# Optimization experiments

Measured on AMD Instinct MI355X. Metric: run time of the kernel, lower is better.

The kernel has to match this reference:

```python
import jax, jax.numpy as jnp
import numpy as np

T = 8192
H = 512
OUT = 2


def _lstm_layer(x, h0, c0, W_ih, W_hh, b_ih, b_hh):
    """Unidirectional LSTM layer, PyTorch gate order (i, f, g, o).
    x: (T, H_in); h0, c0: (H,). Returns (T, H) hidden sequence."""
    b = b_ih + b_hh  # (4H,)
    # Precompute input projections for all timesteps in one GEMM: (T, 4H)
    xg = x @ W_ih.T + b

    def step(carry, xgt):
        h, c = carry
        g = xgt + h @ W_hh.T  # (4H,)
        i, f, gg, o = jnp.split(g, 4)
        i = jax.nn.sigmoid(i)
        f = jax.nn.sigmoid(f)
        gg = jnp.tanh(gg)
        o = jax.nn.sigmoid(o)
        c = f * c + i * gg
        h = o * jnp.tanh(c)
        return (h, c), h

    (_, _), hs = jax.lax.scan(step, (h0, c0), xg)
    return hs


def setup_inputs() -> dict:
    key = jax.random.key(0)
    ks = jax.random.split(key, 16)
    bound = 1.0 / np.sqrt(H)

    def u(k, shape):
        return jax.random.uniform(k, shape, jnp.float32, -bound, bound)

    inp = {
        "tensor_data": jax.random.normal(ks[0], (T, 1, H), jnp.float32),
        "truth_v": jax.random.uniform(ks[1], (T, 1, OUT), jnp.float32),
        "h0": jax.random.normal(ks[2], (2, 1, H), jnp.float32),
        "c0": jax.random.normal(ks[3], (2, 1, H), jnp.float32),
        # layer 0 LSTM params (PyTorch layout: weight_ih (4H, H_in))
        "W_ih0": u(ks[4], (4 * H, H)),
        "W_hh0": u(ks[5], (4 * H, H)),
        "b_ih0": u(ks[6], (4 * H,)),
        "b_hh0": u(ks[7], (4 * H,)),
        # layer 1 LSTM params
        "W_ih1": u(ks[8], (4 * H, H)),
        "W_hh1": u(ks[9], (4 * H, H)),
        "b_ih1": u(ks[10], (4 * H,)),
        "b_hh1": u(ks[11], (4 * H,)),
        # linear head
        "W_head": u(ks[12], (OUT, H)),
        "b_head": u(ks[13], (OUT,)),
    }
    return inp


def reference(tensor_data, truth_v, h0, c0,
              W_ih0, W_hh0, b_ih0, b_hh0,
              W_ih1, W_hh1, b_ih1, b_hh1,
              W_head, b_head):
    x = tensor_data[:, 0, :]  # (T, H), batch = 1
    h1 = _lstm_layer(x, h0[0, 0], c0[0, 0], W_ih0, W_hh0, b_ih0, b_hh0)
    h2 = _lstm_layer(h1, h0[1, 0], c0[1, 0], W_ih1, W_hh1, b_ih1, b_hh1)
    logits = h2 @ W_head.T + b_head  # (T, OUT)
    p = jax.nn.sigmoid(logits)
    y = truth_v[:, 0, :]
    # BCELoss (mean reduction); clamp logs at -100 like torch.nn.BCELoss
    log_p = jnp.maximum(jnp.log(p), -100.0)
    log_1mp = jnp.maximum(jnp.log1p(-p), -100.0)
    loss = -jnp.mean(y * log_p + (1.0 - y) * log_1mp)
    return loss
```

## Files before the change

### kernel.cpp

```cpp
#include <hip/hip_runtime.h>
#include <stdint.h>

#define TSTEPS 8192
#define HDIM 512

typedef unsigned long long ull;

__device__ __forceinline__ ull pack_th(unsigned tag, float v) {
    union { float f; unsigned u; } x; x.f = v;
    return ((ull)tag << 32) | (ull)x.u;
}
__device__ __forceinline__ float unpack_v(ull p) {
    union { unsigned u; float f; } x; x.u = (unsigned)p;
    return x.f;
}

__global__ __attribute__((amdgpu_waves_per_eu(1, 1))) __launch_bounds__(256)
void lstm_fused(
    const float* __restrict__ x,
    const float* __restrict__ Whh0,
    const float* __restrict__ Wih0,
    const float* __restrict__ bih0,
    const float* __restrict__ bhh0,
    const float* __restrict__ Wih1,
    const float* __restrict__ Whh1,
    const float* __restrict__ bih1,
    const float* __restrict__ bhh1,
    const float* __restrict__ h0,
    const float* __restrict__ c0,
    float* __restrict__ h2seq,
    ull* __restrict__ ring0,
    ull* __restrict__ ring1)
{
    const int L2   = (blockIdx.x >= 128) ? 1 : 0;
    const int wb   = L2 ? (int)blockIdx.x - 128 : (int)blockIdx.x;
    const int tid  = threadIdx.x;
    const int wave = tid >> 6;
    const int lane = tid & 63;
    const int j    = wb * 4 + wave;

    float wA[4][8], wB[4][8];
    {
        const float* WA = L2 ? Whh1 : Whh0;
        const float* WB = L2 ? Wih1 : Wih0;
#pragma unroll
        for (int r = 0; r < 4; ++r) {
            const size_t rb = (size_t)(r * HDIM + j) * HDIM + lane;
#pragma unroll
            for (int u = 0; u < 8; ++u) {
                wA[r][u] = WA[rb + 64 * u];
                wB[r][u] = WB[rb + 64 * u];
            }
        }
    }
    float bb[4];
#pragma unroll
    for (int r = 0; r < 4; ++r)
        bb[r] = L2 ? (bih1[r * HDIM + j] + bhh1[r * HDIM + j])
                   : (bih0[r * HDIM + j] + bhh0[r * HDIM + j]);
    float c = c0[(L2 ? HDIM : 0) + j];

    ull* rring = L2 ? ring1 : ring0;

    if (lane == 0)
        __hip_atomic_store(&rring[j], pack_th(1u, h0[(L2 ? HDIM : 0) + j]),
                           __ATOMIC_RELAXED, __HIP_MEMORY_SCOPE_AGENT);

    float fv[8];
    if (!L2) {
#pragma unroll
        for (int u = 0; u < 8; ++u) fv[u] = x[lane + 64 * u];
    } else {
        const ull* s = ring0 + (size_t)1 * HDIM + lane;
        ull p[8]; bool ok;
        do {
            ok = true;
#pragma unroll
            for (int u = 0; u < 8; ++u)
                p[u] = __hip_atomic_load(&s[64 * u], __ATOMIC_RELAXED, __HIP_MEMORY_SCOPE_AGENT);
#pragma unroll
            for (int u = 0; u < 8; ++u) ok &= ((unsigned)(p[u] >> 32) == 2u);
            if (!ok) __builtin_amdgcn_s_sleep(1);
        } while (!ok);
#pragma unroll
        for (int u = 0; u < 8; ++u) fv[u] = unpack_v(p[u]);
    }

    for (int t = 0; t < TSTEPS; ++t) {
        float hv[8];
        {
            const ull* s = rring + (size_t)t * HDIM + lane;
            const unsigned tg = (unsigned)(t + 1);
            ull p[8]; bool ok;
            do {
                ok = true;
#pragma unroll
                for (int u = 0; u < 8; ++u)
                    p[u] = __hip_atomic_load(&s[64 * u], __ATOMIC_RELAXED, __HIP_MEMORY_SCOPE_AGENT);
#pragma unroll
                for (int u = 0; u < 8; ++u) ok &= ((unsigned)(p[u] >> 32) == tg);
                if (!ok) __builtin_amdgcn_s_sleep(1);
            } while (!ok);
#pragma unroll
            for (int u = 0; u < 8; ++u) hv[u] = unpack_v(p[u]);
        }

        float a0 = 0.f, a1 = 0.f, a2 = 0.f, a3 = 0.f;
#pragma unroll
        for (int u = 0; u < 8; ++u) {
            a0 += wA[0][u] * hv[u]; a1 += wA[1][u] * hv[u];
            a2 += wA[2][u] * hv[u]; a3 += wA[3][u] * hv[u];
        }
#pragma unroll
        for (int u = 0; u < 8; ++u) {
            a0 += wB[0][u] * fv[u]; a1 += wB[1][u] * fv[u];
            a2 += wB[2][u] * fv[u]; a3 += wB[3][u] * fv[u];
        }

#pragma unroll
        for (int m = 1; m < 64; m <<= 1) {
            a0 += __shfl_xor(a0, m);
            a1 += __shfl_xor(a1, m);
            a2 += __shfl_xor(a2, m);
            a3 += __shfl_xor(a3, m);
        }

        const float iv = 1.f / (1.f + __expf(-(a0 + bb[0])));
        const float ff = 1.f / (1.f + __expf(-(a1 + bb[1])));
        const float gg = 1.f - 2.f / (__expf(2.f * (a2 + bb[2])) + 1.f);
        const float ov = 1.f / (1.f + __expf(-(a3 + bb[3])));
        c = ff * c + iv * gg;
        const float h = ov * (1.f - 2.f / (__expf(2.f * c) + 1.f));

        if (lane == 0)
            __hip_atomic_store(&rring[(size_t)(t + 1) * HDIM + j],
                               pack_th((unsigned)(t + 2), h),
                               __ATOMIC_RELAXED, __HIP_MEMORY_SCOPE_AGENT);
        if (L2 && lane == 1)
            h2seq[(size_t)t * HDIM + j] = h;

        if (t + 1 < TSTEPS) {
            if (!L2) {
#pragma unroll
                for (int u = 0; u < 8; ++u)
                    fv[u] = x[(size_t)(t + 1) * HDIM + lane + 64 * u];
            } else {
                const ull* s = ring0 + (size_t)(t + 2) * HDIM + lane;
                const unsigned tg = (unsigned)(t + 3);
                ull p[8]; bool ok;
                do {
                    ok = true;
#pragma unroll
                    for (int u = 0; u < 8; ++u)
                        p[u] = __hip_atomic_load(&s[64 * u], __ATOMIC_RELAXED, __HIP_MEMORY_SCOPE_AGENT);
#pragma unroll
                    for (int u = 0; u < 8; ++u) ok &= ((unsigned)(p[u] >> 32) == tg);
                    if (!ok) __builtin_amdgcn_s_sleep(1);
                } while (!ok);
#pragma unroll
                for (int u = 0; u < 8; ++u) fv[u] = unpack_v(p[u]);
            }
        }
    }
}

__global__ __launch_bounds__(256) void head_loss(
    const float* __restrict__ h2,
    const float* __restrict__ Wh,
    const float* __restrict__ bh,
    const float* __restrict__ y,
    float* __restrict__ out)
{
    const int tid  = threadIdx.x;
    const int lane = tid & 63;
    const int wv   = tid >> 6;
    const int gw   = blockIdx.x * 4 + wv;

    float w0[8], w1[8];
#pragma unroll
    for (int u = 0; u < 8; ++u) {
        w0[u] = Wh[lane * 8 + u];
        w1[u] = Wh[HDIM + lane * 8 + u];
    }

    float lsum = 0.f;
    for (int t = gw; t < TSTEPS; t += 1024) {
        const float* hp = h2 + (size_t)t * HDIM + lane * 8;
        float4 hv0 = *(const float4*)&hp[0];
        float4 hv1 = *(const float4*)&hp[4];
        float a0 = hv0.x * w0[0] + hv0.y * w0[1] + hv0.z * w0[2] + hv0.w * w0[3]
                 + hv1.x * w0[4] + hv1.y * w0[5] + hv1.z * w0[6] + hv1.w * w0[7];
        float a1 = hv0.x * w1[0] + hv0.y * w1[1] + hv0.z * w1[2] + hv0.w * w1[3]
                 + hv1.x * w1[4] + hv1.y * w1[5] + hv1.z * w1[6] + hv1.w * w1[7];
#pragma unroll
        for (int m = 1; m < 64; m <<= 1) {
            a0 += __shfl_xor(a0, m);
            a1 += __shfl_xor(a1, m);
        }
        if (lane == 0) {
            const float z0 = a0 + bh[0];
            const float z1 = a1 + bh[1];
            const float p0 = 1.f / (1.f + __expf(-z0));
            const float p1 = 1.f / (1.f + __expf(-z1));
            const float lp0  = fmaxf(__logf(p0), -100.f);
            const float lp1  = fmaxf(__logf(p1), -100.f);
            const float l1p0 = fmaxf(log1pf(-p0), -100.f);
            const float l1p1 = fmaxf(log1pf(-p1), -100.f);
            const float y0 = y[(size_t)t * 2 + 0];
            const float y1 = y[(size_t)t * 2 + 1];
            lsum += y0 * lp0 + (1.f - y0) * l1p0;
            lsum += y1 * lp1 + (1.f - y1) * l1p1;
        }
    }

    __shared__ float red[4];
    if (lane == 0) red[wv] = lsum;
    __syncthreads();
    if (tid == 0) {
        const float ssum = red[0] + red[1] + red[2] + red[3];
        atomicAdd(out, ssum * (-1.f / (float)(TSTEPS * 2)));
    }
}

extern "C" void kernel_launch(void* const* d_in, const int* in_sizes, int n_in,
                              void* d_out, int out_size, void* d_ws, size_t ws_size,
                              hipStream_t stream)
{
    const float* x     = (const float*)d_in[0];
    const float* truth = (const float*)d_in[1];
    const float* h0    = (const float*)d_in[2];
    const float* c0    = (const float*)d_in[3];
    const float* Wih0  = (const float*)d_in[4];
    const float* Whh0  = (const float*)d_in[5];
    const float* bih0  = (const float*)d_in[6];
    const float* bhh0  = (const float*)d_in[7];
    const float* Wih1  = (const float*)d_in[8];
    const float* Whh1  = (const float*)d_in[9];
    const float* bih1  = (const float*)d_in[10];
    const float* bhh1  = (const float*)d_in[11];
    const float* Whead = (const float*)d_in[12];
    const float* bhead = (const float*)d_in[13];

    char* ws = (char*)d_ws;
    ull*   ring0 = (ull*)ws;
    ull*   ring1 = (ull*)(ws + (((size_t)34) << 20));
    float* h2seq = (float*)(ws + (((size_t)68) << 20));

    hipMemsetAsync(d_out, 0, (size_t)out_size * sizeof(float), stream);

    lstm_fused<<<256, 256, 0, stream>>>(x, Whh0, Wih0, bih0, bhh0,
                                        Wih1, Whh1, bih1, bhh1,
                                        h0, c0, h2seq, ring0, ring1);
    head_loss<<<256, 256, 0, stream>>>(h2seq, Whead, bhead, truth, (float*)d_out);
}
```

Baseline: 15.43 ms.

## Restructure LSTM kernel: 64 active blocks, LDS-resident input weights, dual-ring fast polling

Reworks the persistent LSTM kernel so that only 2 of every 8 blocks stay active (one per layer). This is meant to spread the active blocks across separate XCDs or CUs. Each block now handles 16 hidden units, with 16 lanes per unit, and the input-weight slice lives in LDS. The h vector is staged through LDS and broadcast with __syncthreads, and the input-projection partial sum is computed before waiting on the recurrent h. Each h is published to two rings: one read by a fast sc0 vector-load spin without sleeps, and an agent-scope atomic ring used as a fallback. The aim is to shorten the per-step cross-block synchronization latency, at the cost of extra stores, block barriers, and reliance on cache-coherence behaviour of the sc0 path.

```diff
diff --git a/kernel.cpp b/kernel.cpp
--- a/kernel.cpp
+++ b/kernel.cpp
@@ -3,8 +3,12 @@
 
 #define TSTEPS 8192
 #define HDIM 512
+#define LDS_BYTES 135168
+#define WARM 32
+#define FASTK 4096
 
 typedef unsigned long long ull;
+typedef unsigned int uint4v __attribute__((ext_vector_type(4)));
 
 __device__ __forceinline__ ull pack_th(unsigned tag, float v) {
     union { float f; unsigned u; } x; x.f = v;
@@ -14,44 +18,77 @@
     union { unsigned u; float f; } x; x.u = (unsigned)p;
     return x.f;
 }
+__device__ __forceinline__ float bits_f(unsigned u) {
+    union { unsigned u; float f; } x; x.u = u;
+    return x.f;
+}
+__device__ __forceinline__ uint4v sc0_load16(const ull* p) {
+    uint4v r;
+    asm volatile("global_load_dwordx4 %0, %1, off sc0\n\ts_waitcnt vmcnt(0)"
+                 : "=v"(r) : "v"(p) : "memory");
+    return r;
+}
 
 __global__ __attribute__((amdgpu_waves_per_eu(1, 1))) __launch_bounds__(256)
 void lstm_fused(
     const float* __restrict__ x,
-    const float* __restrict__ Whh0,
-    const float* __restrict__ Wih0,
-    const float* __restrict__ bih0,
-    const float* __restrict__ bhh0,
-    const float* __restrict__ Wih1,
-    const float* __restrict__ Whh1,
-    const float* __restrict__ bih1,
-    const float* __restrict__ bhh1,
+    const float* __restrict__ Whh0, const float* __restrict__ Wih0,
+    const float* __restrict__ bih0, const float* __restrict__ bhh0,
+    const float* __restrict__ Wih1, const float* __restrict__ Whh1,
+    const float* __restrict__ bih1, const float* __restrict__ bhh1,
     const float* __restrict__ h0,
     const float* __restrict__ c0,
     float* __restrict__ h2seq,
-    ull* __restrict__ ring0,
-    ull* __restrict__ ring1)
+    ull* __restrict__ r0P, ull* __restrict__ r0Q,
+    ull* __restrict__ r1P, ull* __restrict__ r1Q)
 {
-    const int L2   = (blockIdx.x >= 128) ? 1 : 0;
-    const int wb   = L2 ? (int)blockIdx.x - 128 : (int)blockIdx.x;
+    const int role = (int)blockIdx.x & 7;
+    if (role >= 2) return;
+    const int L2 = role;
+    const int wg = (int)blockIdx.x >> 3;
+
+    extern __shared__ float lds[];
+    float* sWB = lds;
+    float* hA  = lds + 32768;
+    float* hB  = lds + 33280;
+
     const int tid  = threadIdx.x;
     const int wave = tid >> 6;
     const int lane = tid & 63;
-    const int j    = wb * 4 + wave;
-
-    float wA[4][8], wB[4][8];
+    const int uw   = lane >> 4;
+    const int q    = lane & 15;
+    const int ul   = wave * 4 + uw;
+    const int j    = wg * 16 + ul;
+
+    ull* rPs = L2 ? r1P : r0P;
+    ull* rQs = L2 ? r1Q : r0Q;
+
+    if (q == 0) {
+        const float h00 = h0[(L2 ? HDIM : 0) + j];
+        *(volatile ull*)&rPs[j] = pack_th(1u, h00);
+        __hip_atomic_store(&rQs[j], pack_th(1u, h00),
+                           __ATOMIC_RELAXED, __HIP_MEMORY_SCOPE_AGENT);
+    }
+
+    float4 wA[4][8];
     {
         const float* WA = L2 ? Whh1 : Whh0;
+#pragma unroll
+        for (int r = 0; r < 4; ++r) {
+            const float* row = WA + (size_t)(r * HDIM + j) * HDIM + q * 32;
+#pragma unroll
+            for (int i = 0; i < 8; ++i)
+                wA[r][i] = *(const float4*)&row[4 * ((i + q) & 7)];
+        }
+    }
+    {
         const float* WB = L2 ? Wih1 : Wih0;
-#pragma unroll
-        for (int r = 0; r < 4; ++r) {
-            const size_t rb = (size_t)(r * HDIM + j) * HDIM + lane;
-#pragma unroll
-            for (int u = 0; u < 8; ++u) {
-                wA[r][u] = WA[rb + 64 * u];
-                wB[r][u] = WB[rb + 64 * u];
-            }
-        }
+        const int rr = tid >> 2, qq = tid & 3;
+        const int u_r = rr >> 2, g_r = rr & 3;
+        const float4* src = (const float4*)&WB[(size_t)(g_r * HDIM + wg * 16 + u_r) * HDIM + qq * 128];
+        float4* dst = (float4*)&sWB[rr * 512 + qq * 128];
+#pragma unroll
+        for (int i = 0; i < 32; ++i) dst[i] = src[i];
     }
     float bb[4];
 #pragma unroll
@@ -60,71 +97,96 @@
                    : (bih0[r * HDIM + j] + bhh0[r * HDIM + j]);
     float c = c0[(L2 ? HDIM : 0) + j];
 
-    ull* rring = L2 ? ring1 : ring0;
-
-    if (lane == 0)
-        __hip_atomic_store(&rring[j], pack_th(1u, h0[(L2 ? HDIM : 0) + j]),
-                           __ATOMIC_RELAXED, __HIP_MEMORY_SCOPE_AGENT);
-
-    float fv[8];
     if (!L2) {
-#pragma unroll
-        for (int u = 0; u < 8; ++u) fv[u] = x[lane + 64 * u];
+        float2 v = *(const float2*)&x[2 * tid];
+        hB[2 * tid] = v.x; hB[2 * tid + 1] = v.y;
     } else {
-        const ull* s = ring0 + (size_t)1 * HDIM + lane;
-        ull p[8]; bool ok;
+        const ull* s = r0Q + (size_t)1 * HDIM;
+        ull p0, p1;
         do {
-            ok = true;
-#pragma unroll
-            for (int u = 0; u < 8; ++u)
-                p[u] = __hip_atomic_load(&s[64 * u], __ATOMIC_RELAXED, __HIP_MEMORY_SCOPE_AGENT);
-#pragma unroll
-            for (int u = 0; u < 8; ++u) ok &= ((unsigned)(p[u] >> 32) == 2u);
-            if (!ok) __builtin_amdgcn_s_sleep(1);
-        } while (!ok);
-#pragma unroll
-        for (int u = 0; u < 8; ++u) fv[u] = unpack_v(p[u]);
-    }
-
+            p0 = __hip_atomic_load(&s[2 * tid],     __ATOMIC_RELAXED, __HIP_MEMORY_SCOPE_AGENT);
+            p1 = __hip_atomic_load(&s[2 * tid + 1], __ATOMIC_RELAXED, __HIP_MEMORY_SCOPE_AGENT);
+            if ((unsigned)(p0 >> 32) == 2u && (unsigned)(p1 >> 32) == 2u) break;
+            __builtin_amdgcn_s_sleep(1);
+        } while (1);
+        hB[2 * tid] = unpack_v(p0); hB[2 * tid + 1] = unpack_v(p1);
+    }
+    __syncthreads();
+
+    bool fast = true;
     for (int t = 0; t < TSTEPS; ++t) {
-        float hv[8];
+        float pre0 = 0.f, pre1 = 0.f, pre2 = 0.f, pre3 = 0.f;
         {
-            const ull* s = rring + (size_t)t * HDIM + lane;
+            const float* hb = &hB[q * 32];
+            float4 hr[8];
+#pragma unroll
+            for (int i = 0; i < 8; ++i) hr[i] = *(const float4*)&hb[4 * ((i + q) & 7)];
+#pragma unroll
+            for (int r = 0; r < 4; ++r) {
+                const float* wr = &sWB[(ul * 4 + r) * 512 + q * 32];
+                float a = 0.f;
+#pragma unroll
+                for (int i = 0; i < 8; ++i) {
+                    const float4 wq = *(const float4*)&wr[4 * ((i + q) & 7)];
+                    a += wq.x * hr[i].x + wq.y * hr[i].y + wq.z * hr[i].z + wq.w * hr[i].w;
+                }
+                if (r == 0) pre0 = a; else if (r == 1) pre1 = a;
+                else if (r == 2) pre2 = a; else pre3 = a;
+            }
+        }
+        float2 xn;
+        if (!L2 && t + 1 < TSTEPS)
+            xn = *(const float2*)&x[(size_t)(t + 1) * HDIM + 2 * tid];
+
+        {
             const unsigned tg = (unsigned)(t + 1);
-            ull p[8]; bool ok;
-            do {
-                ok = true;
-#pragma unroll
-                for (int u = 0; u < 8; ++u)
-                    p[u] = __hip_atomic_load(&s[64 * u], __ATOMIC_RELAXED, __HIP_MEMORY_SCOPE_AGENT);
-#pragma unroll
-                for (int u = 0; u < 8; ++u) ok &= ((unsigned)(p[u] >> 32) == tg);
-                if (!ok) __builtin_amdgcn_s_sleep(1);
-            } while (!ok);
-#pragma unroll
-            for (int u = 0; u < 8; ++u) hv[u] = unpack_v(p[u]);
-        }
-
-        float a0 = 0.f, a1 = 0.f, a2 = 0.f, a3 = 0.f;
-#pragma unroll
-        for (int u = 0; u < 8; ++u) {
-            a0 += wA[0][u] * hv[u]; a1 += wA[1][u] * hv[u];
-            a2 += wA[2][u] * hv[u]; a3 += wA[3][u] * hv[u];
-        }
-#pragma unroll
-        for (int u = 0; u < 8; ++u) {
-            a0 += wB[0][u] * fv[u]; a1 += wB[1][u] * fv[u];
-            a2 += wB[2][u] * fv[u]; a3 += wB[3][u] * fv[u];
-        }
-
-#pragma unroll
-        for (int m = 1; m < 64; m <<= 1) {
+            float v0, v1; bool have = false;
+            if (fast && t >= WARM) {
+                int tries = 0; uint4v v;
+                do {
+                    v = sc0_load16(&rPs[(size_t)t * HDIM + 2 * tid]);
+                    if (v.y == tg && v.w == tg) { have = true; break; }
+                } while (++tries < FASTK);
+                if (have) { v0 = bits_f(v.x); v1 = bits_f(v.z); }
+                else fast = false;
+            }
+            if (!have) {
+                const ull* s = rQs + (size_t)t * HDIM;
+                ull p0, p1;
+                do {
+                    p0 = __hip_atomic_load(&s[2 * tid],     __ATOMIC_RELAXED, __HIP_MEMORY_SCOPE_AGENT);
+                    p1 = __hip_atomic_load(&s[2 * tid + 1], __ATOMIC_RELAXED, __HIP_MEMORY_SCOPE_AGENT);
+                    if ((unsigned)(p0 >> 32) == tg && (unsigned)(p1 >> 32) == tg) break;
+                    __builtin_amdgcn_s_sleep(1);
+                } while (1);
+                v0 = unpack_v(p0); v1 = unpack_v(p1);
+            }
+            hA[2 * tid] = v0; hA[2 * tid + 1] = v1;
+        }
+        __syncthreads();
+
+        float a0, a1, a2, a3;
+        {
+            const float* ha = &hA[q * 32];
+            float4 hr[8];
+#pragma unroll
+            for (int i = 0; i < 8; ++i) hr[i] = *(const float4*)&ha[4 * ((i + q) & 7)];
+            a0 = pre0; a1 = pre1; a2 = pre2; a3 = pre3;
+#pragma unroll
+            for (int i = 0; i < 8; ++i) {
+                a0 += wA[0][i].x * hr[i].x + wA[0][i].y * hr[i].y + wA[0][i].z * hr[i].z + wA[0][i].w * hr[i].w;
+                a1 += wA[1][i].x * hr[i].x + wA[1][i].y * hr[i].y + wA[1][i].z * hr[i].z + wA[1][i].w * hr[i].w;
+                a2 += wA[2][i].x * hr[i].x + wA[2][i].y * hr[i].y + wA[2][i].z * hr[i].z + wA[2][i].w * hr[i].w;
+                a3 += wA[3][i].x * hr[i].x + wA[3][i].y * hr[i].y + wA[3][i].z * hr[i].z + wA[3][i].w * hr[i].w;
+            }
+        }
+#pragma unroll
+        for (int m = 1; m < 16; m <<= 1) {
             a0 += __shfl_xor(a0, m);
             a1 += __shfl_xor(a1, m);
             a2 += __shfl_xor(a2, m);
             a3 += __shfl_xor(a3, m);
         }
-
         const float iv = 1.f / (1.f + __expf(-(a0 + bb[0])));
         const float ff = 1.f / (1.f + __expf(-(a1 + bb[1])));
         const float gg = 1.f - 2.f / (__expf(2.f * (a2 + bb[2])) + 1.f);
@@ -132,35 +194,31 @@
         c = ff * c + iv * gg;
         const float h = ov * (1.f - 2.f / (__expf(2.f * c) + 1.f));
 
-        if (lane == 0)
-            __hip_atomic_store(&rring[(size_t)(t + 1) * HDIM + j],
-                               pack_th((unsigned)(t + 2), h),
+        if (q == 0) {
+            const ull pk = pack_th((unsigned)(t + 2), h);
+            *(volatile ull*)&rPs[(size_t)(t + 1) * HDIM + j] = pk;
+            __hip_atomic_store(&rQs[(size_t)(t + 1) * HDIM + j], pk,
                                __ATOMIC_RELAXED, __HIP_MEMORY_SCOPE_AGENT);
-        if (L2 && lane == 1)
-            h2seq[(size_t)t * HDIM + j] = h;
+        }
+        if (L2 && q == 1) h2seq[(size_t)t * HDIM + j] = h;
 
         if (t + 1 < TSTEPS) {
             if (!L2) {
-#pragma unroll
-                for (int u = 0; u < 8; ++u)
-                    fv[u] = x[(size_t)(t + 1) * HDIM + lane + 64 * u];
+                hB[2 * tid] = xn.x; hB[2 * tid + 1] = xn.y;
             } else {
-                const ull* s = ring0 + (size_t)(t + 2) * HDIM + lane;
+                const ull* s = r0Q + (size_t)(t + 2) * HDIM;
                 const unsigned tg = (unsigned)(t + 3);
-                ull p[8]; bool ok;
+                ull p0, p1;
                 do {
-                    ok = true;
-#pragma unroll
-                    for (int u = 0; u < 8; ++u)
-                        p[u] = __hip_atomic_load(&s[64 * u], __ATOMIC_RELAXED, __HIP_MEMORY_SCOPE_AGENT);
-#pragma unroll
-                    for (int u = 0; u < 8; ++u) ok &= ((unsigned)(p[u] >> 32) == tg);
-                    if (!ok) __builtin_amdgcn_s_sleep(1);
-                } while (!ok);
-#pragma unroll
-                for (int u = 0; u < 8; ++u) fv[u] = unpack_v(p[u]);
-            }
-        }
+                    p0 = __hip_atomic_load(&s[2 * tid],     __ATOMIC_RELAXED, __HIP_MEMORY_SCOPE_AGENT);
+                    p1 = __hip_atomic_load(&s[2 * tid + 1], __ATOMIC_RELAXED, __HIP_MEMORY_SCOPE_AGENT);
+                    if ((unsigned)(p0 >> 32) == tg && (unsigned)(p1 >> 32) == tg) break;
+                    __builtin_amdgcn_s_sleep(1);
+                } while (1);
+                hB[2 * tid] = unpack_v(p0); hB[2 * tid + 1] = unpack_v(p1);
+            }
+        }
+        __syncthreads();
     }
 }
 
@@ -242,14 +300,20 @@
     const float* bhead = (const float*)d_in[13];
 
     char* ws = (char*)d_ws;
-    ull*   ring0 = (ull*)ws;
-    ull*   ring1 = (ull*)(ws + (((size_t)34) << 20));
-    float* h2seq = (float*)(ws + (((size_t)68) << 20));
+    ull*   r0P   = (ull*)ws;
+    ull*   r0Q   = (ull*)(ws + (((size_t)34)  << 20));
+    ull*   r1P   = (ull*)(ws + (((size_t)68)  << 20));
+    ull*   r1Q   = (ull*)(ws + (((size_t)102) << 20));
+    float* h2seq = (float*)(ws + (((size_t)136) << 20));
 
     hipMemsetAsync(d_out, 0, (size_t)out_size * sizeof(float), stream);
 
-    lstm_fused<<<256, 256, 0, stream>>>(x, Whh0, Wih0, bih0, bhh0,
-                                        Wih1, Whh1, bih1, bhh1,
-                                        h0, c0, h2seq, ring0, ring1);
+    hipFuncSetAttribute((const void*)lstm_fused,
+                        hipFuncAttributeMaxDynamicSharedMemorySize, LDS_BYTES);
+
+    lstm_fused<<<256, 256, LDS_BYTES, stream>>>(x, Whh0, Wih0, bih0, bhh0,
+                                                Wih1, Whh1, bih1, bhh1,
+                                                h0, c0, h2seq,
+                                                r0P, r0Q, r1P, r1Q);
     head_loss<<<256, 256, 0, stream>>>(h2seq, Whead, bhead, truth, (float*)d_out);
 }
```

Result: slower. 27.21 ms (+76.4%).

## Overlap input-path polling and projection with recurrent wait in fused LSTM

Applied to the files above, without the earlier changes.

Moves the input-projection FMAs ahead of the recurrent-state spin-wait, prefetches the next x row early for layer 0, and for layer 1 polls the layer-0 ring for the next input inside the same loop that waits for the recurrent h. It also sleeps only every eighth miss instead of on every miss, to cut wake-up latency on the critical serial dependency. The cost is more atomic-load traffic on the L2/ring from tighter polling, plus extra register use for the prefetched values.

```diff
diff --git a/kernel.cpp b/kernel.cpp
--- a/kernel.cpp
+++ b/kernel.cpp
@@ -87,36 +87,57 @@
     }
 
     for (int t = 0; t < TSTEPS; ++t) {
+        float a0 = 0.f, a1 = 0.f, a2 = 0.f, a3 = 0.f;
+#pragma unroll
+        for (int u = 0; u < 8; ++u) {
+            a0 += wB[0][u] * fv[u]; a1 += wB[1][u] * fv[u];
+            a2 += wB[2][u] * fv[u]; a3 += wB[3][u] * fv[u];
+        }
+        float xn[8];
+        if (!L2) {
+            const int rn = (t + 1 < TSTEPS) ? t + 1 : 0;
+#pragma unroll
+            for (int u = 0; u < 8; ++u)
+                xn[u] = x[(size_t)rn * HDIM + lane + 64 * u];
+        }
+
         float hv[8];
+        ull pf[8];
+        const bool wantF = L2 && (t + 1 < TSTEPS);
+        unsigned doneF = wantF ? 0u : 0xFFu;
+        const ull* sR = rring + (size_t)t * HDIM + lane;
+        const ull* sF = ring0 + (size_t)(t + 2) * HDIM + lane;
+        const unsigned tgR = (unsigned)(t + 1);
+        const unsigned tgF = (unsigned)(t + 3);
         {
-            const ull* s = rring + (size_t)t * HDIM + lane;
-            const unsigned tg = (unsigned)(t + 1);
-            ull p[8]; bool ok;
+            ull pr[8]; bool okR; int miss = 0;
             do {
-                ok = true;
+                okR = true;
 #pragma unroll
                 for (int u = 0; u < 8; ++u)
-                    p[u] = __hip_atomic_load(&s[64 * u], __ATOMIC_RELAXED, __HIP_MEMORY_SCOPE_AGENT);
-#pragma unroll
-                for (int u = 0; u < 8; ++u) ok &= ((unsigned)(p[u] >> 32) == tg);
-                if (!ok) __builtin_amdgcn_s_sleep(1);
-            } while (!ok);
-#pragma unroll
-            for (int u = 0; u < 8; ++u) hv[u] = unpack_v(p[u]);
-        }
-
-        float a0 = 0.f, a1 = 0.f, a2 = 0.f, a3 = 0.f;
+                    pr[u] = __hip_atomic_load(&sR[64 * u], __ATOMIC_RELAXED, __HIP_MEMORY_SCOPE_AGENT);
+                if (doneF != 0xFFu) {
+#pragma unroll
+                    for (int u = 0; u < 8; ++u)
+                        if (!(doneF & (1u << u)))
+                            pf[u] = __hip_atomic_load(&sF[64 * u], __ATOMIC_RELAXED, __HIP_MEMORY_SCOPE_AGENT);
+#pragma unroll
+                    for (int u = 0; u < 8; ++u)
+                        if ((unsigned)(pf[u] >> 32) == tgF) doneF |= (1u << u);
+                }
+#pragma unroll
+                for (int u = 0; u < 8; ++u) okR &= ((unsigned)(pr[u] >> 32) == tgR);
+                if (!okR && ((++miss & 7) == 0)) __builtin_amdgcn_s_sleep(1);
+            } while (!okR);
+#pragma unroll
+            for (int u = 0; u < 8; ++u) hv[u] = unpack_v(pr[u]);
+        }
+
 #pragma unroll
         for (int u = 0; u < 8; ++u) {
             a0 += wA[0][u] * hv[u]; a1 += wA[1][u] * hv[u];
             a2 += wA[2][u] * hv[u]; a3 += wA[3][u] * hv[u];
         }
-#pragma unroll
-        for (int u = 0; u < 8; ++u) {
-            a0 += wB[0][u] * fv[u]; a1 += wB[1][u] * fv[u];
-            a2 += wB[2][u] * fv[u]; a3 += wB[3][u] * fv[u];
-        }
-
 #pragma unroll
         for (int m = 1; m < 64; m <<= 1) {
             a0 += __shfl_xor(a0, m);
@@ -124,7 +145,6 @@
             a2 += __shfl_xor(a2, m);
             a3 += __shfl_xor(a3, m);
         }
-
         const float iv = 1.f / (1.f + __expf(-(a0 + bb[0])));
         const float ff = 1.f / (1.f + __expf(-(a1 + bb[1])));
         const float gg = 1.f - 2.f / (__expf(2.f * (a2 + bb[2])) + 1.f);
@@ -142,23 +162,21 @@
         if (t + 1 < TSTEPS) {
             if (!L2) {
 #pragma unroll
-                for (int u = 0; u < 8; ++u)
-                    fv[u] = x[(size_t)(t + 1) * HDIM + lane + 64 * u];
+                for (int u = 0; u < 8; ++u) fv[u] = xn[u];
             } else {
-                const ull* s = ring0 + (size_t)(t + 2) * HDIM + lane;
-                const unsigned tg = (unsigned)(t + 3);
-                ull p[8]; bool ok;
-                do {
-                    ok = true;
-#pragma unroll
-                    for (int u = 0; u < 8; ++u)
-                        p[u] = __hip_atomic_load(&s[64 * u], __ATOMIC_RELAXED, __HIP_MEMORY_SCOPE_AGENT);
-#pragma unroll
-                    for (int u = 0; u < 8; ++u) ok &= ((unsigned)(p[u] >> 32) == tg);
-                    if (!ok) __builtin_amdgcn_s_sleep(1);
-                } while (!ok);
-#pragma unroll
-                for (int u = 0; u < 8; ++u) fv[u] = unpack_v(p[u]);
+                int miss = 0;
+                while (doneF != 0xFFu) {
+#pragma unroll
+                    for (int u = 0; u < 8; ++u)
+                        if (!(doneF & (1u << u)))
+                            pf[u] = __hip_atomic_load(&sF[64 * u], __ATOMIC_RELAXED, __HIP_MEMORY_SCOPE_AGENT);
+#pragma unroll
+                    for (int u = 0; u < 8; ++u)
+                        if ((unsigned)(pf[u] >> 32) == tgF) doneF |= (1u << u);
+                    if (doneF != 0xFFu && ((++miss & 7) == 0)) __builtin_amdgcn_s_sleep(1);
+                }
+#pragma unroll
+                for (int u = 0; u < 8; ++u) fv[u] = unpack_v(pf[u]);
             }
         }
     }
```

After: 30.40 ms. 1.97x slower.
